# Kernel tuning notes

Hardware: AMD Instinct MI355X
Metric: run time of the kernel (lower is better)

Reference implementation:

```python
import jax, jax.numpy as jnp
import numpy as np

B, IN_UNITS, IN_CH, NUM_UNITS, UNIT_SIZE = 32, 16, 2048, 16, 64
NUM_ITERS = 2


def setup_inputs() -> dict:
    key = jax.random.key(0)
    k1, k2 = jax.random.split(key)
    x = jax.random.normal(k1, (B, IN_UNITS, IN_CH), dtype=jnp.float32)
    W = jax.random.normal(k2, (1, IN_CH, NUM_UNITS, UNIT_SIZE, IN_UNITS), dtype=jnp.float32)
    return {"x": x, "W": W}


def squash(s):
    # torch code sums squared magnitude over dim=2 (the num_units axis) with keepdim
    mag_sq = jnp.sum(s * s, axis=2, keepdims=True)
    mag = jnp.sqrt(mag_sq)
    return mag_sq / (1.0 + mag_sq) * (s / mag)


def reference(x, W):
    # x: (B, in_units, in_channels) -> (B, in_channels, in_units)
    xt = jnp.swapaxes(x, 1, 2)
    # u_hat[b,i,j,k] = sum_u W[0,i,j,k,u] * xt[b,i,u]  -> (B, IC, NU, US)
    u_hat = jnp.einsum('ijku,biu->bijk', W[0], xt)
    b_ij = jnp.zeros((1, IN_CH, NUM_UNITS, 1), dtype=x.dtype)
    v_j = None
    for _ in range(NUM_ITERS):
        # softmax over a singleton trailing dim -> all ones (faithful to source)
        c_ij = jax.nn.softmax(b_ij, axis=-1)  # (1, IC, NU, 1), broadcasts over batch
        s_j = jnp.sum(c_ij[None, ..., 0][0][None].squeeze(0) * 0 + c_ij * u_hat, axis=1, keepdims=True) if False else jnp.sum(c_ij * u_hat, axis=1, keepdims=True)  # (B,1,NU,US)
        v_j = squash(s_j)  # (B,1,NU,US)
        # agreement: <u_hat, v_j> over unit_size, broadcast v_j over in_channels
        u_vj1 = jnp.einsum('bijk,bljk->bij', u_hat, v_j)  # (B, IC, NU)
        u_vj1 = jnp.mean(u_vj1, axis=0, keepdims=True)[..., None]  # (1, IC, NU, 1)
        b_ij = b_ij + u_vj1
    return v_j[:, 0, :, :]  # (B, num_units, unit_size)
```

## Files before the change

kernel.cpp:

```cpp
#include <hip/hip_runtime.h>
#include <hip/hip_bf16.h>

#define B_SZ   32
#define IN_U   16
#define IC     2048
#define NJ     16
#define NK     64

#define ICH    16
#define NCH    (IC/ICH)
#define JG     4
#define NJG    (NJ/JG)
#define SOUT   (B_SZ*NJ*NK)

__global__ __launch_bounds__(256, 3)
void caps_main(const float* __restrict__ x, const float* __restrict__ W,
               float* __restrict__ part) {
    const int tid = threadIdx.x;
    const int p   = blockIdx.x;
    const int jg  = blockIdx.y;
    const int i0  = p * ICH;

    __shared__ float xs[ICH * B_SZ * IN_U];

    #pragma unroll
    for (int it = 0; it < 8; ++it) {
        int q   = it * 256 + tid;
        int row = q >> 2;
        int ip  = q & 3;
        float4 v = *(const float4*)(x + (size_t)row * IC + i0 + 4 * ip);
        int ii = 4 * ip;
        xs[(ii + 0) * 512 + row] = v.x;
        xs[(ii + 1) * 512 + row] = v.y;
        xs[(ii + 2) * 512 + row] = v.z;
        xs[(ii + 3) * 512 + row] = v.w;
    }
    __syncthreads();

    const int k  = tid & 63;
    const int bg = tid >> 6;

    float acc[8][JG];
    #pragma unroll
    for (int b = 0; b < 8; ++b)
        #pragma unroll
        for (int j = 0; j < JG; ++j) acc[b][j] = 0.0f;

    const float* wbase = W + (size_t)i0 * 16384 + (size_t)(jg * JG) * 1024 + k * 16;

    #pragma unroll 1
    for (int ii = 0; ii < ICH; ++ii) {
        const float* wp = wbase + (size_t)ii * 16384;
        float4 w[JG][4];
        #pragma unroll
        for (int j = 0; j < JG; ++j)
            #pragma unroll
            for (int q = 0; q < 4; ++q)
                w[j][q] = *(const float4*)(wp + j * 1024 + q * 4);

        const float* xrow = xs + ii * 512 + bg * 128;
        #pragma unroll
        for (int b = 0; b < 8; ++b) {
            #pragma unroll
            for (int q = 0; q < 4; ++q) {
                float4 xv = *(const float4*)(xrow + b * 16 + q * 4);
                #pragma unroll
                for (int j = 0; j < JG; ++j) {
                    acc[b][j] += w[j][q].x * xv.x;
                    acc[b][j] += w[j][q].y * xv.y;
                    acc[b][j] += w[j][q].z * xv.z;
                    acc[b][j] += w[j][q].w * xv.w;
                }
            }
        }
    }

    float* pp = part + (size_t)p * SOUT + k;
    #pragma unroll
    for (int b = 0; b < 8; ++b)
        #pragma unroll
        for (int j = 0; j < JG; ++j)
            pp[(size_t)((bg * 8 + b) * NJ + jg * JG + j) * NK] = acc[b][j];
}

__global__ __launch_bounds__(1024)
void caps_finish(const float* __restrict__ part, float* __restrict__ out) {
    __shared__ float ls[NJ * NK];
    const int b = blockIdx.x;
    const int t = threadIdx.x;
    const int k = t & 63;

    const size_t base = (size_t)b * (NJ * NK) + t;
    float s = 0.0f;
    #pragma unroll 8
    for (int p = 0; p < NCH; ++p) s += part[(size_t)p * SOUT + base];
    ls[t] = s;
    __syncthreads();

    float msq = 0.0f;
    #pragma unroll
    for (int j = 0; j < NJ; ++j) {
        float v = ls[j * NK + k];
        msq += v * v;
    }
    float mag = sqrtf(msq);
    float f = mag / (1.0f + msq);
    out[base] = s * f;
}

extern "C" void kernel_launch(void* const* d_in, const int* in_sizes, int n_in,
                              void* d_out, int out_size, void* d_ws, size_t ws_size,
                              hipStream_t stream) {
    const float* x = (const float*)d_in[0];
    const float* W = (const float*)d_in[1];
    float* out  = (float*)d_out;
    float* part = (float*)d_ws;

    caps_main  <<<dim3(NCH, NJG), 256,  0, stream>>>(x, W, part);
    caps_finish<<<B_SZ,           1024, 0, stream>>>(part, out);
}
```

Baseline: 213.5 us.

## Compute capsule projection with bf16 MFMA and split-K partials

Replaces the FP32 FMA main kernel with a bf16 MFMA 16x16x32 kernel that treats (in_channel, in_unit) as a 32768-long K dimension, split across 32 K-slices, with a pre-pass that converts x to bf16 in MFMA fragment layout. W is converted to bf16 on the fly in registers. The finish kernel is reshaped to 128 blocks that reduce 32 partials instead of 128. This cuts FP32 ALU work and partial-sum traffic, but bf16 rounding of both operands over a long reduction may loosen accuracy, and with only 512 blocks streaming 128MB of W the kernel may still be bandwidth bound.

```diff
diff --git a/kernel.cpp b/kernel.cpp
--- a/kernel.cpp
+++ b/kernel.cpp
@@ -1,111 +1,115 @@
 #include <hip/hip_runtime.h>
 #include <hip/hip_bf16.h>
 
+
 #define B_SZ   32
-#define IN_U   16
 #define IC     2048
 #define NJ     16
 #define NK     64
+#define SOUT   (B_SZ*NJ*NK)
+#define KSTEPS 1024
+#define KSPLIT 32
+#define SPW    (KSTEPS/KSPLIT)
 
-#define ICH    16
-#define NCH    (IC/ICH)
-#define JG     4
-#define NJG    (NJ/JG)
-#define SOUT   (B_SZ*NJ*NK)
+typedef float v4f __attribute__((ext_vector_type(4)));
+typedef short v8s __attribute__((ext_vector_type(8)));
 
-__global__ __launch_bounds__(256, 3)
-void caps_main(const float* __restrict__ x, const float* __restrict__ W,
+static __device__ inline ushort f2bf(float f) {
+    uint32_t u = __float_as_uint(f);
+    u += 0x7FFFu + ((u >> 16) & 1u);
+    return (ushort)(u >> 16);
+}
+
+__global__ __launch_bounds__(256)
+void caps_xprep(const float* __restrict__ x, ushort* __restrict__ xb) {
+    int gid  = blockIdx.x * 256 + threadIdx.x;
+    int lane = gid & 63;
+    int mt   = (gid >> 6) & 1;
+    int step = gid >> 7;
+    int q    = lane >> 4;
+    int b    = mt * 16 + (lane & 15);
+    int i    = 2 * step + (q >> 1);
+    int u0   = (q & 1) * 8;
+
+    const float* xp = x + (size_t)b * (16 * IC) + (size_t)u0 * IC + i;
+    ushort tmp[8];
+    #pragma unroll
+    for (int jj = 0; jj < 8; ++jj)
+        tmp[jj] = f2bf(xp[(size_t)jj * IC]);
+    *(v8s*)(xb + (size_t)gid * 8) = *(const v8s*)tmp;
+}
+
+__global__ __launch_bounds__(256)
+void caps_mfma(const ushort* __restrict__ xb, const float* __restrict__ W,
                float* __restrict__ part) {
-    const int tid = threadIdx.x;
-    const int p   = blockIdx.x;
-    const int jg  = blockIdx.y;
-    const int i0  = p * ICH;
+    const int tid   = threadIdx.x;
+    const int wv    = tid >> 6;
+    const int lane  = tid & 63;
+    const int j     = blockIdx.x;
+    const int split = blockIdx.y;
+    const int n     = lane & 15;
+    const int q     = lane >> 4;
+    const int step0 = split * SPW;
 
-    __shared__ float xs[ICH * B_SZ * IN_U];
+    v4f acc0 = {0.f, 0.f, 0.f, 0.f};
+    v4f acc1 = {0.f, 0.f, 0.f, 0.f};
 
-    #pragma unroll
-    for (int it = 0; it < 8; ++it) {
-        int q   = it * 256 + tid;
-        int row = q >> 2;
-        int ip  = q & 3;
-        float4 v = *(const float4*)(x + (size_t)row * IC + i0 + 4 * ip);
-        int ii = 4 * ip;
-        xs[(ii + 0) * 512 + row] = v.x;
-        xs[(ii + 1) * 512 + row] = v.y;
-        xs[(ii + 2) * 512 + row] = v.z;
-        xs[(ii + 3) * 512 + row] = v.w;
-    }
-    __syncthreads();
+    const float*  wp = W + (size_t)(2 * step0 + (q >> 1)) * 16384
+                         + (size_t)j * 1024 + (size_t)(wv * 16 + n) * 16 + (q & 1) * 8;
+    const ushort* xp = xb + (size_t)step0 * 1024 + (size_t)lane * 8;
 
-    const int k  = tid & 63;
-    const int bg = tid >> 6;
-
-    float acc[8][JG];
-    #pragma unroll
-    for (int b = 0; b < 8; ++b)
-        #pragma unroll
-        for (int j = 0; j < JG; ++j) acc[b][j] = 0.0f;
-
-    const float* wbase = W + (size_t)i0 * 16384 + (size_t)(jg * JG) * 1024 + k * 16;
-
-    #pragma unroll 1
-    for (int ii = 0; ii < ICH; ++ii) {
-        const float* wp = wbase + (size_t)ii * 16384;
-        float4 w[JG][4];
-        #pragma unroll
-        for (int j = 0; j < JG; ++j)
-            #pragma unroll
-            for (int q = 0; q < 4; ++q)
-                w[j][q] = *(const float4*)(wp + j * 1024 + q * 4);
-
-        const float* xrow = xs + ii * 512 + bg * 128;
-        #pragma unroll
-        for (int b = 0; b < 8; ++b) {
-            #pragma unroll
-            for (int q = 0; q < 4; ++q) {
-                float4 xv = *(const float4*)(xrow + b * 16 + q * 4);
-                #pragma unroll
-                for (int j = 0; j < JG; ++j) {
-                    acc[b][j] += w[j][q].x * xv.x;
-                    acc[b][j] += w[j][q].y * xv.y;
-                    acc[b][j] += w[j][q].z * xv.z;
-                    acc[b][j] += w[j][q].w * xv.w;
-                }
-            }
-        }
+    #pragma unroll 4
+    for (int s = 0; s < SPW; ++s) {
+        float4 w0 = *(const float4*)(wp);
+        float4 w1 = *(const float4*)(wp + 4);
+        v8s a0 = *(const v8s*)(xp);
+        v8s a1 = *(const v8s*)(xp + 512);
+        v8s bb;
+        bb[0] = (short)f2bf(w0.x); bb[1] = (short)f2bf(w0.y);
+        bb[2] = (short)f2bf(w0.z); bb[3] = (short)f2bf(w0.w);
+        bb[4] = (short)f2bf(w1.x); bb[5] = (short)f2bf(w1.y);
+        bb[6] = (short)f2bf(w1.z); bb[7] = (short)f2bf(w1.w);
+        acc0 = __builtin_amdgcn_mfma_f32_16x16x32_bf16(a0, bb, acc0, 0, 0, 0);
+        acc1 = __builtin_amdgcn_mfma_f32_16x16x32_bf16(a1, bb, acc1, 0, 0, 0);
+        wp += 2 * 16384;
+        xp += 1024;
     }
 
-    float* pp = part + (size_t)p * SOUT + k;
+    float* pp = part + (size_t)split * SOUT + (size_t)j * NK + wv * 16 + n;
     #pragma unroll
-    for (int b = 0; b < 8; ++b)
-        #pragma unroll
-        for (int j = 0; j < JG; ++j)
-            pp[(size_t)((bg * 8 + b) * NJ + jg * JG + j) * NK] = acc[b][j];
+    for (int r = 0; r < 4; ++r) {
+        int m = q * 4 + r;
+        pp[(size_t)m * 1024]        = acc0[r];
+        pp[(size_t)(m + 16) * 1024] = acc1[r];
+    }
 }
 
-__global__ __launch_bounds__(1024)
+__global__ __launch_bounds__(256)
 void caps_finish(const float* __restrict__ part, float* __restrict__ out) {
-    __shared__ float ls[NJ * NK];
-    const int b = blockIdx.x;
-    const int t = threadIdx.x;
-    const int k = t & 63;
+    __shared__ float ls[256];
+    const int blk = blockIdx.x;
+    const int b   = blk >> 2;
+    const int k0  = (blk & 3) * 16;
+    const int t   = threadIdx.x;
+    const int jj  = t >> 4;
+    const int kc  = t & 15;
+    const size_t idx = (size_t)b * 1024 + (size_t)jj * NK + k0 + kc;
 
-    const size_t base = (size_t)b * (NJ * NK) + t;
     float s = 0.0f;
     #pragma unroll 8
-    for (int p = 0; p < NCH; ++p) s += part[(size_t)p * SOUT + base];
+    for (int sp = 0; sp < KSPLIT; ++sp)
+        s += part[(size_t)sp * SOUT + idx];
     ls[t] = s;
     __syncthreads();
 
     float msq = 0.0f;
     #pragma unroll
-    for (int j = 0; j < NJ; ++j) {
-        float v = ls[j * NK + k];
+    for (int j2 = 0; j2 < NJ; ++j2) {
+        float v = ls[j2 * 16 + kc];
         msq += v * v;
     }
     float mag = sqrtf(msq);
-    float f = mag / (1.0f + msq);
-    out[base] = s * f;
+    out[idx] = s * (mag / (1.0f + msq));
 }
 
 extern "C" void kernel_launch(void* const* d_in, const int* in_sizes, int n_in,
@@ -114,8 +118,11 @@
     const float* x = (const float*)d_in[0];
     const float* W = (const float*)d_in[1];
     float* out  = (float*)d_out;
-    float* part = (float*)d_ws;
 
-    caps_main  <<<dim3(NCH, NJG), 256,  0, stream>>>(x, W, part);
-    caps_finish<<<B_SZ,           1024, 0, stream>>>(part, out);
+    float*  part = (float*)d_ws;
+    ushort* xb   = (ushort*)(part + (size_t)KSPLIT * SOUT);
+
+    caps_xprep <<<512,               256, 0, stream>>>(x, xb);
+    caps_mfma  <<<dim3(16, KSPLIT),  256, 0, stream>>>(xb, W, part);
+    caps_finish<<<128,               256, 0, stream>>>(part, out);
 }
```

Result: faster. 201.9 us (-5.4%).
